# Performance work log

Hardware: AMD Instinct MI355X
Metric: run time of the kernel (lower is better)

The kernel has to match this reference:

```python
import jax, jax.numpy as jnp
import numpy as np

WINDOW = 5  # window_size from init
C_COARSE = 256
C_FINE = 128


def _gather_windows(fine_nchw, b, lin_idx, stride, pad, w, wc):
    """Extract [M, w*w, C] windows centered on coarse grid cells.

    Equivalent to F.unfold(kernel=w, stride=stride, padding=pad) followed by
    rearrange('n (c ww) l -> n l ww c') and fancy-indexing [b, lin_idx],
    but gathers only the matched windows.
    """
    x = jnp.pad(fine_nchw, ((0, 0), (0, 0), (pad, pad), (pad, pad)))
    x = jnp.transpose(x, (0, 2, 3, 1))  # [N, Hp, Wp, C]
    r = lin_idx // wc
    c = lin_idx % wc
    offs = jnp.arange(w)
    rows = r[:, None] * stride + offs  # [M, w] (start = r*stride - pad, +pad shift)
    cols = c[:, None] * stride + offs  # [M, w]
    patches = x[b[:, None, None], rows[:, :, None], cols[:, None, :]]  # [M, w, w, C]
    return patches.reshape(patches.shape[0], w * w, patches.shape[-1])


def setup_inputs() -> dict:
    key = jax.random.key(0)
    ks = jax.random.split(key, 10)
    N, Hc, Hf, M = 2, 60, 240, 3000
    inp = {
        "coarse_image_feature_1": jax.random.normal(ks[0], (N, Hc * Hc, C_COARSE), jnp.float32),
        "coarse_image_feature_2": jax.random.normal(ks[1], (N, Hc * Hc, C_COARSE), jnp.float32),
        "fine_image_feature_1": jax.random.normal(ks[2], (N, C_FINE, Hf, Hf), jnp.float32),
        "fine_image_feature_2": jax.random.normal(ks[3], (N, C_FINE, Hf, Hf), jnp.float32),
        "batch_indices": jax.random.randint(ks[4], (M,), 0, N),
        "row_indices": jax.random.randint(ks[5], (M,), 0, Hc * Hc),
        "column_indices": jax.random.randint(ks[6], (M,), 0, Hc * Hc),
        "fine_height_width": Hf,
        "coarse_height_width": Hc,
        # learned params (kaiming-normal-ish weights, zero biases)
        "W_dp": jax.random.normal(ks[7], (C_FINE, C_COARSE), jnp.float32) * np.sqrt(2.0 / C_FINE),
        "b_dp": jnp.zeros((C_FINE,), jnp.float32),
        "W_merge": jax.random.normal(ks[8], (C_FINE, 2 * C_FINE), jnp.float32) * np.sqrt(2.0 / C_FINE),
        "b_merge": jnp.zeros((C_FINE,), jnp.float32),
    }
    return inp


def reference(coarse_image_feature_1, coarse_image_feature_2,
              fine_image_feature_1, fine_image_feature_2,
              batch_indices, row_indices, column_indices,
              fine_height_width, coarse_height_width,
              W_dp, b_dp, W_merge, b_merge):
    stride = fine_height_width // coarse_height_width
    pad = WINDOW // 2
    M = batch_indices.shape[0]

    f1 = _gather_windows(fine_image_feature_1, batch_indices, row_indices,
                         stride, pad, WINDOW, coarse_height_width)       # [M, ww, Cf]
    f2 = _gather_windows(fine_image_feature_2, batch_indices, column_indices,
                         stride, pad, WINDOW, coarse_height_width)       # [M, ww, Cf]

    coarse = jnp.concatenate([
        coarse_image_feature_1[batch_indices, row_indices],
        coarse_image_feature_2[batch_indices, column_indices],
    ], axis=0)                                                           # [2M, Cc]
    coarse = coarse @ W_dp.T + b_dp                                      # [2M, Cf]

    fine = jnp.concatenate([f1, f2], axis=0)                             # [2M, ww, Cf]
    combined = jnp.concatenate(
        [fine, jnp.broadcast_to(coarse[:, None, :], fine.shape)], axis=-1)  # [2M, ww, 2Cf]
    merged = combined @ W_merge.T + b_merge                              # [2M, ww, Cf]
    return merged[:M], merged[M:]
```

## Files before the change

kernel.cpp:

```cpp
#include <hip/hip_runtime.h>

#define HF 240
#define HC 60
#define STRIDEF 4
#define PADW 2
#define WIN 5
#define CC 256
#define CF 128
#define NPOS 25
#define NPX (HF*HF)
#define MPB 16
#define TPX 64
#define NSLAB (NPX / TPX)

typedef __bf16 bf16x8 __attribute__((ext_vector_type(8)));
typedef __bf16 bf16x4 __attribute__((ext_vector_type(4)));
typedef float  f32x4  __attribute__((ext_vector_type(4)));

__global__ void k_prep(const float* __restrict__ W_dp, const float* __restrict__ b_dp,
                       const float* __restrict__ W_merge, const float* __restrict__ b_merge,
                       __bf16* __restrict__ Wm1h, float* __restrict__ W_effT,
                       float* __restrict__ b_eff) {
    const int j = blockIdx.x;
    const int k = threadIdx.x;
    const float* wm2 = W_merge + (size_t)j * (2 * CF) + CF;

    float acc = 0.f, accb = 0.f;
    for (int q = 0; q < CF; ++q) {
        const float wq = wm2[q];
        acc  += wq * W_dp[(size_t)q * CC + k];
        accb += wq * b_dp[q];
    }
    W_effT[(size_t)k * CF + j] = acc;

    if (k < CF)
        Wm1h[(size_t)j * CF + k] = (__bf16)W_merge[(size_t)j * (2 * CF) + k];
    if (k == 0)
        b_eff[j] = accb + b_merge[j];
}

__global__ void k_coarse(const float* __restrict__ c1, const float* __restrict__ c2,
                         const int* __restrict__ bidx, const int* __restrict__ ridx,
                         const int* __restrict__ cidx, int M,
                         const float* __restrict__ W_effT, const float* __restrict__ b_eff,
                         float* __restrict__ c_all) {
    const int m0 = blockIdx.x * MPB;
    const int j  = threadIdx.x;
    const int twoM = 2 * M;
    __shared__ float v[MPB * CC];

    const int nm = (twoM - m0) < MPB ? (twoM - m0) : MPB;
    for (int mm = 0; mm < nm; ++mm) {
        int m = m0 + mm;
        const float* src;
        if (m < M) src = c1 + ((size_t)bidx[m] * (HC * HC) + ridx[m]) * CC;
        else       src = c2 + ((size_t)bidx[m - M] * (HC * HC) + cidx[m - M]) * CC;
        v[mm * CC + j]      = src[j];
        v[mm * CC + j + CF] = src[j + CF];
    }
    __syncthreads();

    float acc[MPB];
    const float be = b_eff[j];
    #pragma unroll
    for (int mm = 0; mm < MPB; ++mm) acc[mm] = be;

    for (int k = 0; k < CC; k += 4) {
        float w0 = W_effT[(k + 0) * CF + j];
        float w1 = W_effT[(k + 1) * CF + j];
        float w2 = W_effT[(k + 2) * CF + j];
        float w3 = W_effT[(k + 3) * CF + j];
        #pragma unroll
        for (int mm = 0; mm < MPB; ++mm) {
            const f32x4 vv = *(const f32x4*)&v[mm * CC + k];
            acc[mm] += w0 * vv.x + w1 * vv.y + w2 * vv.z + w3 * vv.w;
        }
    }
    for (int mm = 0; mm < nm; ++mm)
        c_all[(size_t)(m0 + mm) * CF + j] = acc[mm];
}

__global__ __launch_bounds__(256, 6) void k_tgemm(
    const float* __restrict__ f1, const float* __restrict__ f2,
    const __bf16* __restrict__ Wm1h, __bf16* __restrict__ V) {

    int slab = blockIdx.x;
    {
        const int q = NSLAB / 8, r = NSLAB % 8;
        const int xcd = slab & 7, off = slab >> 3;
        slab = (xcd < r ? xcd * (q + 1) : r * (q + 1) + (xcd - r) * q) + off;
    }
    const int slot = blockIdx.y;
    const float* src = (slot >= 2 ? f2 : f1) + (size_t)(slot & 1) * CF * NPX;
    const int px0 = slab * TPX;
    const int t  = threadIdx.x;
    const int l  = t & 63;
    const int w  = t >> 6;
    const int lo16 = l & 15;
    const int hi   = l >> 4;

    __shared__ __attribute__((aligned(16))) float chkf[2][32 * TPX];

    const int q4 = lo16 * 4;

#define STAGE(c, b)                                                           \
    {                                                                         \
        _Pragma("unroll")                                                     \
        for (int ii = 0; ii < 2; ++ii) {                                      \
            const int i  = w * 2 + ii;                        \
            const int ch = (c) * 32 + i * 4 + hi;                             \
            const int pxg = q4 ^ (((ch >> 3) & 3) << 4);                      \
            const float* gp = src + (size_t)ch * NPX + px0 + pxg;             \
            __builtin_amdgcn_global_load_lds(                                 \
                (const __attribute__((address_space(1))) void*)gp,            \
                (__attribute__((address_space(3))) void*)&chkf[b][i * 256],   \
                16, 0, 0);                                                    \
        }                                                                     \
    }

    f32x4 acc[4][2];
    #pragma unroll
    for (int mt = 0; mt < 4; ++mt) {
        acc[mt][0] = (f32x4){0.f, 0.f, 0.f, 0.f};
        acc[mt][1] = (f32x4){0.f, 0.f, 0.f, 0.f};
    }

    STAGE(0, 0);

    #pragma unroll
    for (int c = 0; c < 4; ++c) {
        const int b = c & 1;
        if (c < 3) STAGE(c + 1, b ^ 1);
        __syncthreads();

        const bf16x8 bf0 = *reinterpret_cast<const bf16x8*>(
            Wm1h + (size_t)(w * 32 + 2 * lo16 + 0) * CF + c * 32 + hi * 8);
        const bf16x8 bf1 = *reinterpret_cast<const bf16x8*>(
            Wm1h + (size_t)(w * 32 + 2 * lo16 + 1) * CF + c * 32 + hi * 8);

        #pragma unroll
        for (int mt = 0; mt < 4; ++mt) {
            const int pxr = (mt * 16 + lo16) ^ (hi << 4);
            bf16x8 a;
            #pragma unroll
            for (int e = 0; e < 8; ++e)
                a[e] = (__bf16)chkf[b][(hi * 8 + e) * TPX + pxr];
            acc[mt][0] = __builtin_amdgcn_mfma_f32_16x16x32_bf16(a, bf0, acc[mt][0], 0, 0, 0);
            acc[mt][1] = __builtin_amdgcn_mfma_f32_16x16x32_bf16(a, bf1, acc[mt][1], 0, 0, 0);
        }
        __syncthreads();
    }
#undef STAGE

    uint* Vp = (uint*)(V + ((size_t)slot * NPX + px0) * CF);
    const int dcol = w * 16 + lo16;
    #pragma unroll
    for (int mt = 0; mt < 4; ++mt) {
        #pragma unroll
        for (int reg = 0; reg < 4; ++reg) {
            const int px = mt * 16 + hi * 4 + reg;
            union { uint u; __bf16 h[2]; } cv;
            cv.h[0] = (__bf16)acc[mt][0][reg];
            cv.h[1] = (__bf16)acc[mt][1][reg];
            Vp[(size_t)px * 64 + dcol] = cv.u;
        }
    }
}

__global__ __launch_bounds__(256) void k_gather(
    const __bf16* __restrict__ V,
    const int* __restrict__ bidx, const int* __restrict__ ridx,
    const int* __restrict__ cidx, int M,
    const float* __restrict__ c_all, float* __restrict__ out) {

    const int m = blockIdx.x;
    const int t = threadIdx.x;
    const int g  = t >> 5;
    const int l32 = t & 31;

    int b, lin, ii;
    if (m < M) { ii = 0; b = bidx[m];     lin = ridx[m]; }
    else       { ii = 1; b = bidx[m - M]; lin = cidx[m - M]; }
    const int slot = ii * 2 + b;
    const int r  = lin / HC, c = lin - r * HC;
    const int y0 = r * STRIDEF - PADW;
    const int x0 = c * STRIDEF - PADW;

    const f32x4 c4 = *reinterpret_cast<const f32x4*>(c_all + (size_t)m * CF + l32 * 4);
    const __bf16* Vb = V + (size_t)slot * NPX * CF;
    float* ob = out + (size_t)m * (NPOS * CF) + l32 * 4;

    #pragma unroll
    for (int pass = 0; pass < 4; ++pass) {
        const int p = pass * 8 + g;
        if (p < NPOS) {
            const int wy = (p * 13) >> 6;
            const int wx = p - wy * WIN;
            const int y = y0 + wy, x = x0 + wx;
            f32x4 o = c4;
            if (y >= 0 && x >= 0) {
                const bf16x4 v = *reinterpret_cast<const bf16x4*>(Vb + (size_t)(y * HF + x) * CF + l32 * 4);
                o.x += (float)v.x; o.y += (float)v.y; o.z += (float)v.z; o.w += (float)v.w;
            }
            __builtin_nontemporal_store(o, reinterpret_cast<f32x4*>(ob + (size_t)p * CF));
        }
    }
}

__global__ __launch_bounds__(256) void k_main_direct(
    const float* __restrict__ f1, const float* __restrict__ f2,
    const int* __restrict__ bidx, const int* __restrict__ ridx,
    const int* __restrict__ cidx, int M,
    const __bf16* __restrict__ Wm1h, const float* __restrict__ c_all,
    float* __restrict__ out) {

    const int m = blockIdx.x;
    const int t = threadIdx.x;
    const int l    = t & 63;
    const int wv   = t >> 6;
    const int lo16 = l & 15;
    const int hi   = l >> 4;

    __shared__ __bf16 patch[32 * CF];

    bf16x8 bfrag[2][4];
    #pragma unroll
    for (int nt2 = 0; nt2 < 2; ++nt2) {
        const int j = wv * 32 + nt2 * 16 + lo16;
        #pragma unroll
        for (int kt = 0; kt < 4; ++kt)
            bfrag[nt2][kt] = *reinterpret_cast<const bf16x8*>(Wm1h + (size_t)j * CF + kt * 32 + hi * 8);
    }

    const float* img; int b, lin;
    if (m < M) { img = f1; b = bidx[m];     lin = ridx[m]; }
    else       { img = f2; b = bidx[m - M]; lin = cidx[m - M]; }
    const int r  = lin / HC, c = lin - r * HC;
    const int y0 = r * STRIDEF - PADW;
    const int x0 = c * STRIDEF - PADW;

    for (int task = t; task < CF * WIN; task += 256) {
        const int ch = task / WIN;
        const int wy = task - ch * WIN;
        const int y  = y0 + wy;
        const bool yok = (y >= 0);
        const float* rowp = img + (((size_t)b * CF + ch) * HF + (yok ? y : 0)) * HF;
        #pragma unroll
        for (int wx = 0; wx < WIN; ++wx) {
            const int x = x0 + wx;
            const float val = (yok && x >= 0) ? rowp[x] : 0.f;
            const int pos = wy * WIN + wx;
            patch[pos * CF + (ch ^ ((pos & 7) << 3))] = (__bf16)val;
        }
    }
    __syncthreads();

    f32x4 acc[2][2];
    #pragma unroll
    for (int mt = 0; mt < 2; ++mt)
        #pragma unroll
        for (int nt2 = 0; nt2 < 2; ++nt2)
            acc[mt][nt2] = (f32x4){0.f, 0.f, 0.f, 0.f};

    const int swz = (lo16 & 7) << 3;
    #pragma unroll
    for (int kt = 0; kt < 4; ++kt) {
        const int koff = (kt * 32 + hi * 8) ^ swz;
        bf16x8 a0 = *reinterpret_cast<const bf16x8*>(&patch[ lo16       * CF + koff]);
        bf16x8 a1 = *reinterpret_cast<const bf16x8*>(&patch[(16 + lo16) * CF + koff]);
        #pragma unroll
        for (int nt2 = 0; nt2 < 2; ++nt2) {
            acc[0][nt2] = __builtin_amdgcn_mfma_f32_16x16x32_bf16(a0, bfrag[nt2][kt], acc[0][nt2], 0, 0, 0);
            acc[1][nt2] = __builtin_amdgcn_mfma_f32_16x16x32_bf16(a1, bfrag[nt2][kt], acc[1][nt2], 0, 0, 0);
        }
    }

    float* ob = out + (size_t)m * (NPOS * CF);
    #pragma unroll
    for (int nt2 = 0; nt2 < 2; ++nt2) {
        const int j  = wv * 32 + nt2 * 16 + lo16;
        const float cv = c_all[(size_t)m * CF + j];
        #pragma unroll
        for (int mt = 0; mt < 2; ++mt) {
            #pragma unroll
            for (int reg = 0; reg < 4; ++reg) {
                const int p = mt * 16 + hi * 4 + reg;
                if (p < NPOS)
                    ob[(size_t)p * CF + j] = acc[mt][nt2][reg] + cv;
            }
        }
    }
}

extern "C" void kernel_launch(void* const* d_in, const int* in_sizes, int n_in,
                              void* d_out, int out_size, void* d_ws, size_t ws_size,
                              hipStream_t stream) {
    const float* c1      = (const float*)d_in[0];
    const float* c2      = (const float*)d_in[1];
    const float* f1      = (const float*)d_in[2];
    const float* f2      = (const float*)d_in[3];
    const int*   bidx    = (const int*)d_in[4];
    const int*   ridx    = (const int*)d_in[5];
    const int*   cidx    = (const int*)d_in[6];
    const float* W_dp    = (const float*)d_in[9];
    const float* b_dp    = (const float*)d_in[10];
    const float* W_merge = (const float*)d_in[11];
    const float* b_merge = (const float*)d_in[12];
    const int M = in_sizes[4];

    char* ws = (char*)d_ws;
    __bf16* Wm1h  = (__bf16*)(ws);
    float* W_effT = (float*)(ws + (64 << 10));
    float* b_eff  = (float*)(ws + (192 << 10));
    float* c_all  = (float*)(ws + (256 << 10));
    __bf16* V     = (__bf16*)(ws + (4 << 20));

    const size_t need_V = (size_t)(4 << 20) + (size_t)4 * NPX * CF * 2;

    hipLaunchKernelGGL(k_prep, dim3(CF), dim3(CC), 0, stream,
                       W_dp, b_dp, W_merge, b_merge, Wm1h, W_effT, b_eff);
    hipLaunchKernelGGL(k_coarse, dim3((2 * M + MPB - 1) / MPB), dim3(CF), 0, stream,
                       c1, c2, bidx, ridx, cidx, M, W_effT, b_eff, c_all);

    if (ws_size >= need_V) {
        hipLaunchKernelGGL(k_tgemm, dim3(NSLAB, 4), dim3(256), 0, stream,
                           f1, f2, Wm1h, V);
        hipLaunchKernelGGL(k_gather, dim3(2 * M), dim3(256), 0, stream,
                           V, bidx, ridx, cidx, M, c_all, (float*)d_out);
    } else {
        hipLaunchKernelGGL(k_main_direct, dim3(2 * M), dim3(256), 0, stream,
                           f1, f2, bidx, ridx, cidx, M, Wm1h, c_all, (float*)d_out);
    }
}
```

Before: 93.89 us.

## Fuse window gather into dense transform GEMM via per-slab scatter index lists

Removes the bf16 intermediate V buffer and the separate gather kernel. A new index kernel bins each (match, window position) pair into per-64-pixel slab lists with atomics. The GEMM kernel stages its fp32 result tile in a larger shared buffer and writes the output rows for its listed entries directly, adding the coarse term. Out-of-bounds padded positions are filled by a small edge kernel. The trade-offs are more shared memory (occupancy lowered to 4), atomic contention, and a fixed per-slab capacity that silently drops entries if a slab is overfull.

```diff
diff --git a/kernel.cpp b/kernel.cpp
--- a/kernel.cpp
+++ b/kernel.cpp
@@ -12,19 +12,24 @@
 #define MPB 16
 #define TPX 64
 #define NSLAB (NPX / TPX)
+#define CAP 256
 
 typedef __bf16 bf16x8 __attribute__((ext_vector_type(8)));
 typedef __bf16 bf16x4 __attribute__((ext_vector_type(4)));
 typedef float  f32x4  __attribute__((ext_vector_type(4)));
+typedef float  f32x2  __attribute__((ext_vector_type(2)));
 
 __global__ void k_prep(const float* __restrict__ W_dp, const float* __restrict__ b_dp,
                        const float* __restrict__ W_merge, const float* __restrict__ b_merge,
                        __bf16* __restrict__ Wm1h, float* __restrict__ W_effT,
-                       float* __restrict__ b_eff) {
+                       float* __restrict__ b_eff, uint* __restrict__ cnt) {
     const int j = blockIdx.x;
     const int k = threadIdx.x;
+
+    const int tid = j * 256 + k;
+    if (tid < 4 * NSLAB) cnt[tid] = 0;
+
     const float* wm2 = W_merge + (size_t)j * (2 * CF) + CF;
-
     float acc = 0.f, accb = 0.f;
     for (int q = 0; q < CF; ++q) {
         const float wq = wm2[q];
@@ -80,9 +85,35 @@
         c_all[(size_t)(m0 + mm) * CF + j] = acc[mm];
 }
 
-__global__ __launch_bounds__(256, 6) void k_tgemm(
+__global__ __launch_bounds__(256) void k_index(
+    const int* __restrict__ bidx, const int* __restrict__ ridx,
+    const int* __restrict__ cidx, int M,
+    uint* __restrict__ cnt, uint* __restrict__ entries) {
+    const int tid = blockIdx.x * 256 + threadIdx.x;
+    const int m = tid >> 5, pp = tid & 31;
+    if (m >= 2 * M || pp >= NPOS) return;
+    int b, lin;
+    if (m < M) { b = bidx[m];     lin = ridx[m]; }
+    else       { b = bidx[m - M]; lin = cidx[m - M]; }
+    const int slot = (m < M ? 0 : 2) + b;
+    const int r = lin / HC, c = lin - r * HC;
+    const int wy = pp / WIN, wx = pp - wy * WIN;
+    const int y = r * STRIDEF - PADW + wy;
+    const int x = c * STRIDEF - PADW + wx;
+    if (y < 0 || x < 0) return;
+    const int pixel = y * HF + x;
+    const int cslab = slot * NSLAB + pixel / TPX;
+    const uint idx = atomicAdd(&cnt[cslab], 1u);
+    if (idx < CAP)
+        entries[(size_t)cslab * CAP + idx] =
+            ((uint)m << 11) | ((uint)pp << 6) | (uint)(pixel % TPX);
+}
+
+__global__ __launch_bounds__(256, 4) void k_tgemm(
     const float* __restrict__ f1, const float* __restrict__ f2,
-    const __bf16* __restrict__ Wm1h, __bf16* __restrict__ V) {
+    const __bf16* __restrict__ Wm1h, const float* __restrict__ c_all,
+    const uint* __restrict__ cnt, const uint* __restrict__ entries,
+    float* __restrict__ out) {
 
     int slab = blockIdx.x;
     {
@@ -99,7 +130,7 @@
     const int lo16 = l & 15;
     const int hi   = l >> 4;
 
-    __shared__ __attribute__((aligned(16))) float chkf[2][32 * TPX];
+    __shared__ __attribute__((aligned(16))) float smem[TPX * CF];
 
     const int q4 = lo16 * 4;
 
@@ -113,7 +144,8 @@
             const float* gp = src + (size_t)ch * NPX + px0 + pxg;             \
             __builtin_amdgcn_global_load_lds(                                 \
                 (const __attribute__((address_space(1))) void*)gp,            \
-                (__attribute__((address_space(3))) void*)&chkf[b][i * 256],   \
+                (__attribute__((address_space(3))) void*)                     \
+                    &smem[(b) * 2048 + i * 256],                              \
                 16, 0, 0);                                                    \
         }                                                                     \
     }
@@ -144,7 +176,7 @@
             bf16x8 a;
             #pragma unroll
             for (int e = 0; e < 8; ++e)
-                a[e] = (__bf16)chkf[b][(hi * 8 + e) * TPX + pxr];
+                a[e] = (__bf16)smem[b * 2048 + (hi * 8 + e) * TPX + pxr];
             acc[mt][0] = __builtin_amdgcn_mfma_f32_16x16x32_bf16(a, bf0, acc[mt][0], 0, 0, 0);
             acc[mt][1] = __builtin_amdgcn_mfma_f32_16x16x32_bf16(a, bf1, acc[mt][1], 0, 0, 0);
         }
@@ -152,58 +184,54 @@
     }
 #undef STAGE
 
-    uint* Vp = (uint*)(V + ((size_t)slot * NPX + px0) * CF);
-    const int dcol = w * 16 + lo16;
     #pragma unroll
     for (int mt = 0; mt < 4; ++mt) {
         #pragma unroll
         for (int reg = 0; reg < 4; ++reg) {
             const int px = mt * 16 + hi * 4 + reg;
-            union { uint u; __bf16 h[2]; } cv;
-            cv.h[0] = (__bf16)acc[mt][0][reg];
-            cv.h[1] = (__bf16)acc[mt][1][reg];
-            Vp[(size_t)px * 64 + dcol] = cv.u;
-        }
-    }
-}
-
-__global__ __launch_bounds__(256) void k_gather(
-    const __bf16* __restrict__ V,
+            smem[px * CF + w * 32 + 2 * lo16 + 0] = acc[mt][0][reg];
+            smem[px * CF + w * 32 + 2 * lo16 + 1] = acc[mt][1][reg];
+        }
+    }
+    __syncthreads();
+
+    const int cslab = slot * NSLAB + slab;
+    int count = (int)cnt[cslab];
+    if (count > CAP) count = CAP;
+    const uint* ep = entries + (size_t)cslab * CAP;
+    for (int i = w; i < count; i += 4) {
+        const uint e = ep[i];
+        const int pxl = e & 63;
+        const int p   = (e >> 6) & 31;
+        const int m   = e >> 11;
+        const f32x2 v  = *(const f32x2*)&smem[pxl * CF + 2 * l];
+        const f32x2 cv = *(const f32x2*)(c_all + (size_t)m * CF + 2 * l);
+        f32x2 o = { v.x + cv.x, v.y + cv.y };
+        *(f32x2*)(out + ((size_t)m * NPOS + p) * CF + 2 * l) = o;
+    }
+}
+
+__global__ __launch_bounds__(256) void k_edge(
     const int* __restrict__ bidx, const int* __restrict__ ridx,
     const int* __restrict__ cidx, int M,
     const float* __restrict__ c_all, float* __restrict__ out) {
-
     const int m = blockIdx.x;
     const int t = threadIdx.x;
-    const int g  = t >> 5;
-    const int l32 = t & 31;
-
-    int b, lin, ii;
-    if (m < M) { ii = 0; b = bidx[m];     lin = ridx[m]; }
-    else       { ii = 1; b = bidx[m - M]; lin = cidx[m - M]; }
-    const int slot = ii * 2 + b;
-    const int r  = lin / HC, c = lin - r * HC;
+    const int wv = t >> 6, l = t & 63;
+    int b, lin;
+    if (m < M) { b = bidx[m];     lin = ridx[m]; }
+    else       { b = bidx[m - M]; lin = cidx[m - M]; }
+    (void)b;
+    const int r = lin / HC, c = lin - r * HC;
     const int y0 = r * STRIDEF - PADW;
     const int x0 = c * STRIDEF - PADW;
-
-    const f32x4 c4 = *reinterpret_cast<const f32x4*>(c_all + (size_t)m * CF + l32 * 4);
-    const __bf16* Vb = V + (size_t)slot * NPX * CF;
-    float* ob = out + (size_t)m * (NPOS * CF) + l32 * 4;
-
-    #pragma unroll
-    for (int pass = 0; pass < 4; ++pass) {
-        const int p = pass * 8 + g;
-        if (p < NPOS) {
-            const int wy = (p * 13) >> 6;
-            const int wx = p - wy * WIN;
-            const int y = y0 + wy, x = x0 + wx;
-            f32x4 o = c4;
-            if (y >= 0 && x >= 0) {
-                const bf16x4 v = *reinterpret_cast<const bf16x4*>(Vb + (size_t)(y * HF + x) * CF + l32 * 4);
-                o.x += (float)v.x; o.y += (float)v.y; o.z += (float)v.z; o.w += (float)v.w;
-            }
-            __builtin_nontemporal_store(o, reinterpret_cast<f32x4*>(ob + (size_t)p * CF));
-        }
+    if (y0 >= 0 && x0 >= 0) return;
+    const f32x2 cv = *(const f32x2*)(c_all + (size_t)m * CF + 2 * l);
+    for (int p = wv; p < NPOS; p += 4) {
+        const int wy = (p * 13) >> 6;
+        const int wx = p - wy * WIN;
+        if (y0 + wy < 0 || x0 + wx < 0)
+            *(f32x2*)(out + ((size_t)m * NPOS + p) * CF + 2 * l) = cv;
     }
 }
 
@@ -309,24 +337,28 @@
     const int M = in_sizes[4];
 
     char* ws = (char*)d_ws;
-    __bf16* Wm1h  = (__bf16*)(ws);
-    float* W_effT = (float*)(ws + (64 << 10));
-    float* b_eff  = (float*)(ws + (192 << 10));
-    float* c_all  = (float*)(ws + (256 << 10));
-    __bf16* V     = (__bf16*)(ws + (4 << 20));
-
-    const size_t need_V = (size_t)(4 << 20) + (size_t)4 * NPX * CF * 2;
+    __bf16* Wm1h   = (__bf16*)(ws);
+    float*  W_effT = (float*)(ws + (64 << 10));
+    float*  b_eff  = (float*)(ws + (192 << 10));
+    float*  c_all  = (float*)(ws + (256 << 10));
+    uint*   cnt    = (uint*)(ws + (4 << 20));
+    uint*   entr   = (uint*)(ws + (5 << 20));
+
+    const size_t need = (size_t)(5 << 20) + (size_t)4 * NSLAB * CAP * 4;
 
     hipLaunchKernelGGL(k_prep, dim3(CF), dim3(CC), 0, stream,
-                       W_dp, b_dp, W_merge, b_merge, Wm1h, W_effT, b_eff);
+                       W_dp, b_dp, W_merge, b_merge, Wm1h, W_effT, b_eff, cnt);
     hipLaunchKernelGGL(k_coarse, dim3((2 * M + MPB - 1) / MPB), dim3(CF), 0, stream,
                        c1, c2, bidx, ridx, cidx, M, W_effT, b_eff, c_all);
 
-    if (ws_size >= need_V) {
+    if (ws_size >= need) {
+        const int nidx = (2 * M * 32 + 255) / 256;
+        hipLaunchKernelGGL(k_index, dim3(nidx), dim3(256), 0, stream,
+                           bidx, ridx, cidx, M, cnt, entr);
         hipLaunchKernelGGL(k_tgemm, dim3(NSLAB, 4), dim3(256), 0, stream,
-                           f1, f2, Wm1h, V);
-        hipLaunchKernelGGL(k_gather, dim3(2 * M), dim3(256), 0, stream,
-                           V, bidx, ridx, cidx, M, c_all, (float*)d_out);
+                           f1, f2, Wm1h, c_all, cnt, entr, (float*)d_out);
+        hipLaunchKernelGGL(k_edge, dim3(2 * M), dim3(256), 0, stream,
+                           bidx, ridx, cidx, M, c_all, (float*)d_out);
     } else {
         hipLaunchKernelGGL(k_main_direct, dim3(2 * M), dim3(256), 0, stream,
                            f1, f2, bidx, ridx, cidx, M, Wm1h, c_all, (float*)d_out);
```

Result: slower. 113.9 us (+21.3%).
